# Kernel optimization log

Hardware: AMD Instinct MI355X
Metric: run time of the kernel (lower is better)

## Reference

```python
import jax, jax.numpy as jnp
import numpy as np


def setup_inputs() -> dict:
    key = jax.random.key(0)
    ks = jax.random.split(key, 5)
    B, S, H = 64, 1024, 1024
    scale = 1.0 / np.sqrt(H)
    return {
        "decoder_hidden": jax.random.normal(ks[0], (B, H), jnp.float32),
        "encoder_outputs": jax.random.normal(ks[1], (B, S, H), jnp.float32),
        "W1": jax.random.normal(ks[2], (H, H), jnp.float32) * scale,
        "W2": jax.random.normal(ks[3], (H, H), jnp.float32) * scale,
        "v": jax.random.normal(ks[4], (H,), jnp.float32) * scale,
    }


def reference(decoder_hidden, encoder_outputs, W1, W2, v):
    # W1 @ decoder_hidden: [B, H] computed once, broadcast over src_len
    dh_proj = jnp.einsum("bh,oh->bo", decoder_hidden, W1)          # [B, H]
    enc_proj = jnp.einsum("bsh,oh->bso", encoder_outputs, W2)      # [B, S, H]
    energy = jnp.tanh(dh_proj[:, None, :] + enc_proj)              # [B, S, H]
    scores = jnp.einsum("bsh,h->bs", energy, v)                    # [B, S]
    attention_weights = jax.nn.softmax(scores, axis=-1)            # [B, S]
    context = jnp.einsum("bs,bsh->bh", attention_weights, encoder_outputs)
    return (context, attention_weights)
```

## Files before the change

kernel.cpp:

```cpp
#include <hip/hip_runtime.h>
#include <hip/hip_bf16.h>
#include <cmath>

#define Hdim 1024
#define Bdim 64
#define Sdim 1024

typedef __attribute__((ext_vector_type(4))) float f32x4;
typedef __attribute__((ext_vector_type(8))) short s16x8;
typedef __attribute__((ext_vector_type(4))) unsigned int u32x4;

static __device__ __forceinline__ unsigned short f2bf(float f) {
  unsigned int u = __builtin_bit_cast(unsigned int, f);
  unsigned int r = (u + 0x7fffu + ((u >> 16) & 1u)) >> 16;
  return (unsigned short)r;
}


static __device__ __forceinline__ void stage_rows64(const float* __restrict__ src,
                                                    unsigned short* As, int tid) {
  #pragma unroll 4
  for (int i = 0; i < 32; ++i) {
    int c = tid + i * 256;
    int row = c >> 7;
    int k8 = (c & 127) << 3;
    const float4* p = reinterpret_cast<const float4*>(src + row * Hdim + k8);
    float4 a = p[0];
    float4 b = p[1];
    union { unsigned short us[8]; u32x4 v; } pk;
    pk.us[0] = f2bf(a.x); pk.us[1] = f2bf(a.y); pk.us[2] = f2bf(a.z); pk.us[3] = f2bf(a.w);
    pk.us[4] = f2bf(b.x); pk.us[5] = f2bf(b.y); pk.us[6] = f2bf(b.z); pk.us[7] = f2bf(b.w);
    int idx = row * Hdim + (k8 ^ ((row & 7) << 3));
    *reinterpret_cast<u32x4*>(&As[idx]) = pk.v;
  }
}

static __device__ __forceinline__ s16x8 lda_full(const unsigned short* As, int row, int k) {
  int idx = row * Hdim + (k ^ ((row & 7) << 3));
  return *reinterpret_cast<const s16x8*>(&As[idx]);
}

static __device__ __forceinline__ s16x8 ldb_g(const unsigned short* __restrict__ Wb,
                                              const float* __restrict__ Wf,
                                              int use_bf, int o, int k) {
  if (use_bf) {
    return *reinterpret_cast<const s16x8*>(&Wb[o * Hdim + k]);
  } else {
    const float4* p = reinterpret_cast<const float4*>(Wf + o * Hdim + k);
    float4 a = p[0];
    float4 b = p[1];
    union { unsigned short us[8]; s16x8 v; } pk;
    pk.us[0] = f2bf(a.x); pk.us[1] = f2bf(a.y); pk.us[2] = f2bf(a.z); pk.us[3] = f2bf(a.w);
    pk.us[4] = f2bf(b.x); pk.us[5] = f2bf(b.y); pk.us[6] = f2bf(b.z); pk.us[7] = f2bf(b.w);
    return pk.v;
  }
}

__global__ void cast_bf16_kernel(const float* __restrict__ src,
                                 unsigned short* __restrict__ dst) {
  int i = blockIdx.x * 256 + threadIdx.x;
  const float4* p = reinterpret_cast<const float4*>(src) + i * 2;
  float4 a = p[0];
  float4 b = p[1];
  union { unsigned short us[8]; u32x4 v; } pk;
  pk.us[0] = f2bf(a.x); pk.us[1] = f2bf(a.y); pk.us[2] = f2bf(a.z); pk.us[3] = f2bf(a.w);
  pk.us[4] = f2bf(b.x); pk.us[5] = f2bf(b.y); pk.us[6] = f2bf(b.z); pk.us[7] = f2bf(b.w);
  *reinterpret_cast<u32x4*>(dst + i * 8) = pk.v;
}

__global__ __launch_bounds__(256, 1) void proj_kernel(
    const float* __restrict__ dh, const float* __restrict__ W1f,
    const unsigned short* __restrict__ W1b, float* __restrict__ out, int use_bf) {
  __shared__ unsigned short As[64 * Hdim];
  int tid = threadIdx.x;
  stage_rows64(dh, As, tid);
  __syncthreads();
  int w = tid >> 6, lane = tid & 63;
  int lo = lane & 15, hi = lane >> 4;
  int o = blockIdx.x * 16 + lo;
  f32x4 acc = {0.f, 0.f, 0.f, 0.f};
  for (int k0 = 0; k0 < Hdim; k0 += 32) {
    int k = k0 + hi * 8;
    s16x8 bfrag = ldb_g(W1b, W1f, use_bf, o, k);
    s16x8 afrag = lda_full(As, w * 16 + lo, k);
    acc = __builtin_amdgcn_mfma_f32_16x16x32_bf16(afrag, bfrag, acc, 0, 0, 0);
  }
  #pragma unroll
  for (int r = 0; r < 4; ++r)
    out[(w * 16 + hi * 4 + r) * Hdim + o] = acc[r];
}

#define SBM 128
#define SBN 128
#define SBK 64

__global__ __launch_bounds__(256, 3) void score_mfma_kernel(
    const unsigned short* __restrict__ encb,
    const unsigned short* __restrict__ W2b,
    const float* __restrict__ dhp, const float* __restrict__ v,
    float* __restrict__ scores) {
  __shared__ unsigned short As[SBM * SBK];
  __shared__ unsigned short Bs[SBN * SBK];
  __shared__ float ssum[SBM];
  int tid = threadIdx.x;
  int bid = blockIdx.x;
  int swz = (bid & 7) * 512 + (bid >> 3);
  int mp = swz >> 3;
  int np = swz & 7;
  int row0 = mp * SBM;
  int b = row0 >> 10;
  int w = tid >> 6, lane = tid & 63;
  int wr = w >> 1, wc = w & 1;
  int lo = lane & 15, hi = lane >> 4;

  if (tid < SBM) ssum[tid] = 0.f;

  const unsigned short* gA[4];
  const unsigned short* gB[4];
  #pragma unroll
  for (int i = 0; i < 4; ++i) {
    int d = i * 256 + tid;
    int row = d >> 3, c = d & 7;
    int gc = c ^ (row & 7);
    gA[i] = encb + (size_t)(row0 + row) * Hdim + gc * 8;
    gB[i] = W2b + (size_t)(np * SBN + row) * Hdim + gc * 8;
  }

  f32x4 acc[4][4] = {};

  for (int t = 0; t < 16; ++t) {
    __syncthreads();
    #pragma unroll
    for (int i = 0; i < 4; ++i) {
      int dwv = i * 256 + w * 64;
      __builtin_amdgcn_global_load_lds(
          (const __attribute__((address_space(1))) unsigned int*)gA[i],
          (__attribute__((address_space(3))) unsigned int*)(As + dwv * 8), 16, 0, 0);
      __builtin_amdgcn_global_load_lds(
          (const __attribute__((address_space(1))) unsigned int*)gB[i],
          (__attribute__((address_space(3))) unsigned int*)(Bs + dwv * 8), 16, 0, 0);
      gA[i] += SBK;
      gB[i] += SBK;
    }
    asm volatile("s_waitcnt vmcnt(0)" ::: "memory");
    __syncthreads();

    const char* Ab = (const char*)As;
    const char* Bb = (const char*)Bs;
    #pragma unroll
    for (int ks = 0; ks < 2; ++ks) {
      int kb = (ks * 32 + hi * 8) * 2;
      s16x8 af[4], bf[4];
      #pragma unroll
      for (int m = 0; m < 4; ++m) {
        int row = wr * 64 + m * 16 + lo;
        af[m] = *reinterpret_cast<const s16x8*>(Ab + row * (SBK * 2) + (kb ^ ((row & 7) << 4)));
      }
      #pragma unroll
      for (int n = 0; n < 4; ++n) {
        int row = wc * 64 + n * 16 + lo;
        bf[n] = *reinterpret_cast<const s16x8*>(Bb + row * (SBK * 2) + (kb ^ ((row & 7) << 4)));
      }
      #pragma unroll
      for (int m = 0; m < 4; ++m)
        #pragma unroll
        for (int n = 0; n < 4; ++n)
          acc[m][n] = __builtin_amdgcn_mfma_f32_16x16x32_bf16(af[m], bf[n], acc[m][n], 0, 0, 0);
    }
  }

  float psum[4][4] = {};
  #pragma unroll
  for (int n = 0; n < 4; ++n) {
    int o = np * SBN + wc * 64 + n * 16 + lo;
    float dv = dhp[b * Hdim + o];
    float vv = v[o];
    #pragma unroll
    for (int m = 0; m < 4; ++m)
      #pragma unroll
      for (int r = 0; r < 4; ++r)
        psum[m][r] += tanhf(acc[m][n][r] + dv) * vv;
  }
  #pragma unroll
  for (int mask = 1; mask < 16; mask <<= 1)
    #pragma unroll
    for (int m = 0; m < 4; ++m)
      #pragma unroll
      for (int r = 0; r < 4; ++r)
        psum[m][r] += __shfl_xor(psum[m][r], mask, 64);
  if (lo == 0) {
    #pragma unroll
    for (int m = 0; m < 4; ++m)
      #pragma unroll
      for (int r = 0; r < 4; ++r)
        atomicAdd(&ssum[wr * 64 + m * 16 + hi * 4 + r], psum[m][r]);
  }
  __syncthreads();
  if (tid < SBM) atomicAdd(&scores[row0 + tid], ssum[tid]);
}

#define BKt 64

__global__ __launch_bounds__(256, 3) void score_kernel(
    const float* __restrict__ enc, const float* __restrict__ W2f,
    const unsigned short* __restrict__ W2b, const float* __restrict__ dhp,
    const float* __restrict__ v, float* __restrict__ scores, int use_bf) {
  __shared__ unsigned short As[64 * BKt];
  int tid = threadIdx.x;
  int bid = blockIdx.x;
  int f = (bid & 7) * 512 + (bid >> 3);
  int rg = f >> 2;
  int oc = f & 3;
  int row0 = rg * 64;
  int b = row0 >> 10;
  int w = tid >> 6, lane = tid & 63;
  int lo = lane & 15, hi = lane >> 4;
  int n0 = oc * 256 + w * 64;

  const unsigned short* pB[4];
  const float* pBf[4];
  #pragma unroll
  for (int n = 0; n < 4; ++n) {
    int o = n0 + n * 16 + lo;
    pB[n]  = W2b + (size_t)o * Hdim + hi * 8;
    pBf[n] = W2f + (size_t)o * Hdim + hi * 8;
  }

  f32x4 acc[4][4] = {};

  for (int t = 0; t < 16; ++t) {
    int k0 = t * BKt;
    __syncthreads();
    #pragma unroll
    for (int cc = 0; cc < 2; ++cc) {
      int c = tid + cc * 256;
      int row = c >> 3;
      int j = c & 7;
      const float4* p = reinterpret_cast<const float4*>(
          enc + (size_t)(row0 + row) * Hdim + k0 + j * 8);
      float4 a = p[0];
      float4 bb = p[1];
      union { unsigned short us[8]; u32x4 v4; } pk;
      pk.us[0] = f2bf(a.x);  pk.us[1] = f2bf(a.y);  pk.us[2] = f2bf(a.z);  pk.us[3] = f2bf(a.w);
      pk.us[4] = f2bf(bb.x); pk.us[5] = f2bf(bb.y); pk.us[6] = f2bf(bb.z); pk.us[7] = f2bf(bb.w);
      int idx = row * BKt + ((j * 8) ^ ((row & 7) << 3));
      *reinterpret_cast<u32x4*>(&As[idx]) = pk.v4;
    }
    __syncthreads();

    #pragma unroll
    for (int ks = 0; ks < 2; ++ks) {
      s16x8 bfrag[4];
      #pragma unroll
      for (int n = 0; n < 4; ++n) {
        if (use_bf) {
          bfrag[n] = *reinterpret_cast<const s16x8*>(pB[n] + ks * 32);
        } else {
          const float4* p = reinterpret_cast<const float4*>(pBf[n] + ks * 32);
          float4 a = p[0];
          float4 bb = p[1];
          union { unsigned short us[8]; s16x8 v4; } pk;
          pk.us[0] = f2bf(a.x);  pk.us[1] = f2bf(a.y);  pk.us[2] = f2bf(a.z);  pk.us[3] = f2bf(a.w);
          pk.us[4] = f2bf(bb.x); pk.us[5] = f2bf(bb.y); pk.us[6] = f2bf(bb.z); pk.us[7] = f2bf(bb.w);
          bfrag[n] = pk.v4;
        }
      }
      #pragma unroll
      for (int m = 0; m < 4; ++m) {
        int kk = ks * 32 + hi * 8;
        s16x8 afrag = *reinterpret_cast<const s16x8*>(
            &As[(m * 16 + lo) * BKt + (kk ^ ((lo & 7) << 3))]);
        #pragma unroll
        for (int n = 0; n < 4; ++n)
          acc[m][n] = __builtin_amdgcn_mfma_f32_16x16x32_bf16(afrag, bfrag[n], acc[m][n], 0, 0, 0);
      }
    }
    #pragma unroll
    for (int n = 0; n < 4; ++n) { pB[n] += BKt; pBf[n] += BKt; }
  }

  float psum[4][4] = {};
  #pragma unroll
  for (int n = 0; n < 4; ++n) {
    int o = n0 + n * 16 + lo;
    float dv = dhp[b * Hdim + o];
    float vv = v[o];
    #pragma unroll
    for (int m = 0; m < 4; ++m)
      #pragma unroll
      for (int r = 0; r < 4; ++r)
        psum[m][r] += tanhf(acc[m][n][r] + dv) * vv;
  }
  #pragma unroll
  for (int mask = 1; mask < 16; mask <<= 1)
    #pragma unroll
    for (int m = 0; m < 4; ++m)
      #pragma unroll
      for (int r = 0; r < 4; ++r)
        psum[m][r] += __shfl_xor(psum[m][r], mask, 64);
  if (lo == 0) {
    #pragma unroll
    for (int m = 0; m < 4; ++m)
      #pragma unroll
      for (int r = 0; r < 4; ++r)
        atomicAdd(&scores[row0 + m * 16 + hi * 4 + r], psum[m][r]);
  }
}

__global__ __launch_bounds__(256, 1) void softmax_kernel(float* __restrict__ attn) {
  __shared__ float redm[4];
  __shared__ float reds[4];
  int b = blockIdx.x, tid = threadIdx.x;
  float4 x = *reinterpret_cast<float4*>(attn + b * Sdim + tid * 4);
  float m = fmaxf(fmaxf(x.x, x.y), fmaxf(x.z, x.w));
  #pragma unroll
  for (int mask = 1; mask < 64; mask <<= 1) m = fmaxf(m, __shfl_xor(m, mask, 64));
  if ((tid & 63) == 0) redm[tid >> 6] = m;
  __syncthreads();
  m = fmaxf(fmaxf(redm[0], redm[1]), fmaxf(redm[2], redm[3]));
  float4 e;
  e.x = expf(x.x - m); e.y = expf(x.y - m); e.z = expf(x.z - m); e.w = expf(x.w - m);
  float s = e.x + e.y + e.z + e.w;
  #pragma unroll
  for (int mask = 1; mask < 64; mask <<= 1) s += __shfl_xor(s, mask, 64);
  if ((tid & 63) == 0) reds[tid >> 6] = s;
  __syncthreads();
  s = reds[0] + reds[1] + reds[2] + reds[3];
  float inv = 1.f / s;
  e.x *= inv; e.y *= inv; e.z *= inv; e.w *= inv;
  *reinterpret_cast<float4*>(attn + b * Sdim + tid * 4) = e;
}

__global__ __launch_bounds__(256, 1) void context_kernel(
    const float* __restrict__ enc, const float* __restrict__ attn,
    float* __restrict__ ctx) {
  int b = blockIdx.x >> 3;
  int chunk = blockIdx.x & 7;
  int tid = threadIdx.x;
  int h0 = tid * 4;
  const float* ebase = enc + ((size_t)(b * Sdim + chunk * 128)) * Hdim + h0;
  const float* abase = attn + b * Sdim + chunk * 128;
  float4 acc = {0.f, 0.f, 0.f, 0.f};
  #pragma unroll 4
  for (int s = 0; s < 128; ++s) {
    float wgt = abase[s];
    float4 ev = *reinterpret_cast<const float4*>(ebase + (size_t)s * Hdim);
    acc.x += wgt * ev.x; acc.y += wgt * ev.y; acc.z += wgt * ev.z; acc.w += wgt * ev.w;
  }
  float* c = ctx + b * Hdim + h0;
  atomicAdd(c + 0, acc.x);
  atomicAdd(c + 1, acc.y);
  atomicAdd(c + 2, acc.z);
  atomicAdd(c + 3, acc.w);
}

extern "C" void kernel_launch(void* const* d_in, const int* in_sizes, int n_in,
                              void* d_out, int out_size, void* d_ws, size_t ws_size,
                              hipStream_t stream) {
  const float* dh  = (const float*)d_in[0];
  const float* enc = (const float*)d_in[1];
  const float* W1  = (const float*)d_in[2];
  const float* W2  = (const float*)d_in[3];
  const float* v   = (const float*)d_in[4];
  float* out_ctx  = (float*)d_out;
  float* out_attn = out_ctx + Bdim * Hdim;

  int use_bf = (ws_size >= 4ull * 1024 * 1024) ? 1 : 0;
  int big_ws = (ws_size >= 133ull * 1024 * 1024) ? 1 : 0;
  unsigned short* W1b  = (unsigned short*)d_ws;
  unsigned short* W2b  = W1b + 1024 * 1024;
  unsigned short* encb = W2b + 1024 * 1024;

  if (use_bf) {
    cast_bf16_kernel<<<512, 256, 0, stream>>>(W1, W1b);
    cast_bf16_kernel<<<512, 256, 0, stream>>>(W2, W2b);
  }
  if (big_ws) {
    cast_bf16_kernel<<<32768, 256, 0, stream>>>(enc, encb);
  }

  proj_kernel<<<64, 256, 0, stream>>>(dh, W1, W1b, out_ctx, use_bf);

  hipMemsetAsync(out_attn, 0, (size_t)Bdim * Sdim * sizeof(float), stream);
  if (big_ws) {
    score_mfma_kernel<<<4096, 256, 0, stream>>>(encb, W2b, out_ctx, v, out_attn);
  } else {
    score_kernel<<<4096, 256, 0, stream>>>(enc, W2, W2b, out_ctx, v, out_attn, use_bf);
  }

  softmax_kernel<<<Bdim, 256, 0, stream>>>(out_attn);

  hipMemsetAsync(out_ctx, 0, (size_t)Bdim * Hdim * sizeof(float), stream);
  context_kernel<<<512, 256, 0, stream>>>(enc, out_attn, out_ctx);
}
```

Before: 330.9 us.

## Double-buffer score GEMM, use fast exp2 tanh, read bf16 encoder in context

The score MFMA kernel now uses two LDS buffers, so the global-to-LDS load of the next K tile overlaps the MFMAs on the current one. tanhf is replaced by an exp2/rcp formulation in both score kernels, and the context reduction reads the bf16 copy of the encoder instead of fp32, halving its traffic, with twice as many blocks. The costs are doubled LDS per block (which may cut occupancy from 3 blocks per CU), reduced tanh accuracy, and bf16 rounding of encoder values in the context output.

```diff
diff --git a/kernel.cpp b/kernel.cpp
--- a/kernel.cpp
+++ b/kernel.cpp
@@ -15,6 +15,12 @@
   unsigned int r = (u + 0x7fffu + ((u >> 16) & 1u)) >> 16;
   return (unsigned short)r;
 }
+
+static __device__ __forceinline__ float bf2f(unsigned short u) {
+  return __builtin_bit_cast(float, (unsigned int)u << 16);
+}
+
+#define TANH_C 2.885390081777927f
 
 
 static __device__ __forceinline__ void stage_rows64(const float* __restrict__ src,
@@ -99,8 +105,8 @@
     const unsigned short* __restrict__ W2b,
     const float* __restrict__ dhp, const float* __restrict__ v,
     float* __restrict__ scores) {
-  __shared__ unsigned short As[SBM * SBK];
-  __shared__ unsigned short Bs[SBN * SBK];
+  __shared__ unsigned short As[2][SBM * SBK];
+  __shared__ unsigned short Bs[2][SBN * SBK];
   __shared__ float ssum[SBM];
   int tid = threadIdx.x;
   int bid = blockIdx.x;
@@ -126,27 +132,33 @@
     gB[i] = W2b + (size_t)(np * SBN + row) * Hdim + gc * 8;
   }
 
-  f32x4 acc[4][4] = {};
-
-  for (int t = 0; t < 16; ++t) {
-    __syncthreads();
+  auto STAGE = [&](int buf) {
     #pragma unroll
     for (int i = 0; i < 4; ++i) {
       int dwv = i * 256 + w * 64;
       __builtin_amdgcn_global_load_lds(
           (const __attribute__((address_space(1))) unsigned int*)gA[i],
-          (__attribute__((address_space(3))) unsigned int*)(As + dwv * 8), 16, 0, 0);
+          (__attribute__((address_space(3))) unsigned int*)(&As[buf][dwv * 8]), 16, 0, 0);
       __builtin_amdgcn_global_load_lds(
           (const __attribute__((address_space(1))) unsigned int*)gB[i],
-          (__attribute__((address_space(3))) unsigned int*)(Bs + dwv * 8), 16, 0, 0);
+          (__attribute__((address_space(3))) unsigned int*)(&Bs[buf][dwv * 8]), 16, 0, 0);
       gA[i] += SBK;
       gB[i] += SBK;
     }
-    asm volatile("s_waitcnt vmcnt(0)" ::: "memory");
-    __syncthreads();
-
-    const char* Ab = (const char*)As;
-    const char* Bb = (const char*)Bs;
+  };
+
+  f32x4 acc[4][4] = {};
+
+  STAGE(0);
+  asm volatile("s_waitcnt vmcnt(0)" ::: "memory");
+  __syncthreads();
+
+  int cur = 0;
+  for (int t = 0; t < 16; ++t) {
+    if (t < 15) STAGE(cur ^ 1);
+
+    const char* Ab = (const char*)As[cur];
+    const char* Bb = (const char*)Bs[cur];
     #pragma unroll
     for (int ks = 0; ks < 2; ++ks) {
       int kb = (ks * 32 + hi * 8) * 2;
@@ -167,6 +179,9 @@
         for (int n = 0; n < 4; ++n)
           acc[m][n] = __builtin_amdgcn_mfma_f32_16x16x32_bf16(af[m], bf[n], acc[m][n], 0, 0, 0);
     }
+    asm volatile("s_waitcnt vmcnt(0)" ::: "memory");
+    __syncthreads();
+    cur ^= 1;
   }
 
   float psum[4][4] = {};
@@ -175,11 +190,16 @@
     int o = np * SBN + wc * 64 + n * 16 + lo;
     float dv = dhp[b * Hdim + o];
     float vv = v[o];
-    #pragma unroll
-    for (int m = 0; m < 4; ++m)
-      #pragma unroll
-      for (int r = 0; r < 4; ++r)
-        psum[m][r] += tanhf(acc[m][n][r] + dv) * vv;
+    float vv2 = 2.f * vv;
+    #pragma unroll
+    for (int m = 0; m < 4; ++m)
+      #pragma unroll
+      for (int r = 0; r < 4; ++r) {
+        float x = acc[m][n][r] + dv;
+        float e2 = __builtin_amdgcn_exp2f(x * TANH_C);
+        float rc = __builtin_amdgcn_rcpf(1.f + e2);
+        psum[m][r] += vv - vv2 * rc;
+      }
   }
   #pragma unroll
   for (int mask = 1; mask < 16; mask <<= 1)
@@ -285,11 +305,16 @@
     int o = n0 + n * 16 + lo;
     float dv = dhp[b * Hdim + o];
     float vv = v[o];
-    #pragma unroll
-    for (int m = 0; m < 4; ++m)
-      #pragma unroll
-      for (int r = 0; r < 4; ++r)
-        psum[m][r] += tanhf(acc[m][n][r] + dv) * vv;
+    float vv2 = 2.f * vv;
+    #pragma unroll
+    for (int m = 0; m < 4; ++m)
+      #pragma unroll
+      for (int r = 0; r < 4; ++r) {
+        float x = acc[m][n][r] + dv;
+        float e2 = __builtin_amdgcn_exp2f(x * TANH_C);
+        float rc = __builtin_amdgcn_rcpf(1.f + e2);
+        psum[m][r] += vv - vv2 * rc;
+      }
   }
   #pragma unroll
   for (int mask = 1; mask < 16; mask <<= 1)
@@ -329,6 +354,32 @@
   float inv = 1.f / s;
   e.x *= inv; e.y *= inv; e.z *= inv; e.w *= inv;
   *reinterpret_cast<float4*>(attn + b * Sdim + tid * 4) = e;
+}
+
+__global__ __launch_bounds__(256, 1) void context_bf_kernel(
+    const unsigned short* __restrict__ encb, const float* __restrict__ attn,
+    float* __restrict__ ctx) {
+  int b = blockIdx.x >> 4;
+  int chunk = blockIdx.x & 15;
+  int tid = threadIdx.x;
+  int h0 = tid * 4;
+  const unsigned short* ebase = encb + ((size_t)(b * Sdim + chunk * 64)) * Hdim + h0;
+  const float* abase = attn + b * Sdim + chunk * 64;
+  float4 acc = {0.f, 0.f, 0.f, 0.f};
+  #pragma unroll 4
+  for (int s = 0; s < 64; ++s) {
+    float wgt = abase[s];
+    ushort4 ev = *reinterpret_cast<const ushort4*>(ebase + (size_t)s * Hdim);
+    acc.x += wgt * bf2f(ev.x);
+    acc.y += wgt * bf2f(ev.y);
+    acc.z += wgt * bf2f(ev.z);
+    acc.w += wgt * bf2f(ev.w);
+  }
+  float* c = ctx + b * Hdim + h0;
+  atomicAdd(c + 0, acc.x);
+  atomicAdd(c + 1, acc.y);
+  atomicAdd(c + 2, acc.z);
+  atomicAdd(c + 3, acc.w);
 }
 
 __global__ __launch_bounds__(256, 1) void context_kernel(
@@ -391,5 +442,9 @@
   softmax_kernel<<<Bdim, 256, 0, stream>>>(out_attn);
 
   hipMemsetAsync(out_ctx, 0, (size_t)Bdim * Hdim * sizeof(float), stream);
-  context_kernel<<<512, 256, 0, stream>>>(enc, out_attn, out_ctx);
-}
+  if (big_ws) {
+    context_bf_kernel<<<1024, 256, 0, stream>>>(encb, out_attn, out_ctx);
+  } else {
+    context_kernel<<<512, 256, 0, stream>>>(enc, out_attn, out_ctx);
+  }
+}
```

Result: no change. 325.0 us (-1.8%).
